# Performance work log

Measured on AMD Instinct MI355X. Metric: run time of the kernel, lower is better.

Reference implementation:

```python
import jax, jax.numpy as jnp
import numpy as np

N_NODES = 50000
N_EDGES = 1250000
D = 64
EPS = 1e-07


def setup_inputs() -> dict:
    key = jax.random.key(0)
    ks = jax.random.split(key, 10)
    return {
        "node_feats": jax.random.normal(ks[0], (N_NODES, D), jnp.float32),
        "emb0": jax.random.normal(ks[1], (8, D), jnp.float32),
        "emb1": jax.random.normal(ks[2], (4, D), jnp.float32),
        "W": jax.random.normal(ks[3], (D, D), jnp.float32) / np.sqrt(D),
        "b": jnp.zeros((D,), jnp.float32),
        "beta": jnp.ones((1,), jnp.float32),
        "scale": jnp.ones((1,), jnp.float32),
        "src": jax.random.randint(ks[4], (N_EDGES,), 0, N_NODES),
        "dst": jax.random.randint(ks[5], (N_EDGES,), 0, N_NODES),
        "edge_feat0": jax.random.randint(ks[6], (N_EDGES,), 0, 8),
        "edge_feat1": jax.random.randint(ks[7], (N_EDGES,), 0, 4),
    }


def reference(node_feats, emb0, emb1, W, b, beta, scale, src, dst, edge_feat0, edge_feat1):
    n = node_feats.shape[0]
    # edge embeddings summed over categorical feature types
    e = emb0[edge_feat0] + emb1[edge_feat1]              # [E, D]
    # u_add_e then relu + eps
    m = jnp.maximum(node_feats[src] + e, 0.0) + EPS      # [E, D]
    # edge softmax over edges sharing the same destination (per feature dim)
    logits = m * beta                                    # [E, D]
    mx = jax.ops.segment_max(logits, dst, num_segments=n)
    ex = jnp.exp(logits - mx[dst])
    denom = jax.ops.segment_sum(ex, dst, num_segments=n)
    a = ex / denom[dst]                                  # [E, D]
    # scatter-sum aggregation of m * a to destination nodes
    msg = jax.ops.segment_sum(m * a, dst, num_segments=n)  # [N, D]
    # MessageNorm: L2-normalize msg, rescale by ||node_feats|| * scale
    msg_unit = msg / jnp.maximum(
        jnp.linalg.norm(msg, axis=-1, keepdims=True), 1e-12)
    feats_norm = jnp.linalg.norm(node_feats, axis=-1, keepdims=True)
    msg = msg_unit * feats_norm * scale
    # residual + single-layer MLP
    feats = node_feats + msg
    return feats @ W + b
```

## Files before the change

### kernel.cpp

```cpp
#include <hip/hip_runtime.h>

#define NN 50000
#define NE 1250000
#define DD 64
#define KRF 1563
#define BSH 5
#define SCAPF 1024
#define SCSHF 10


__global__ __launch_bounds__(512) void k_part(
    const int4* __restrict__ src4, const int4* __restrict__ dst4,
    const int4* __restrict__ ef04, const int4* __restrict__ ef14,
    const float* __restrict__ W, float* __restrict__ Wt,
    int* __restrict__ rcur, unsigned* __restrict__ staging)
{
    __shared__ int hist[KRF], rbase[KRF], cur[KRF];
    const int t  = threadIdx.x;
    const int gb = blockIdx.x;

    for (int i = t; i < KRF; i += 512) { hist[i] = 0; cur[i] = 0; }
    if (gb == 0)
        for (int i = t; i < 4096; i += 512)
            Wt[(i & 63) * DD + (i >> 6)] = W[i];
    __syncthreads();

    unsigned pay[4];
    int rr[4];
#pragma unroll
    for (int u = 0; u < 4; ++u) rr[u] = -1;

    const int i4 = gb * 512 + t;
    if (i4 < NE / 4) {
        const int4 s  = src4[i4], d = dst4[i4];
        const int4 f0 = ef04[i4], f1 = ef14[i4];
        const int ds[4] = {d.x, d.y, d.z, d.w};
        const int ss[4] = {s.x, s.y, s.z, s.w};
        const int a0[4] = {f0.x, f0.y, f0.z, f0.w};
        const int a1[4] = {f1.x, f1.y, f1.z, f1.w};
#pragma unroll
        for (int u = 0; u < 4; ++u) {
            rr[u]  = ds[u] >> BSH;
            pay[u] = (unsigned)ss[u] | ((unsigned)(a1[u] * 8 + a0[u]) << 16)
                     | ((unsigned)(ds[u] & 31) << 21);
        }
    }
#pragma unroll
    for (int u = 0; u < 4; ++u)
        if (rr[u] >= 0) atomicAdd(&hist[rr[u]], 1);
    __syncthreads();

    for (int i = t; i < KRF; i += 512) {
        const int h = hist[i];
        if (h) rbase[i] = atomicAdd(&rcur[i], h);
    }
    __syncthreads();

#pragma unroll
    for (int u = 0; u < 4; ++u) {
        if (rr[u] >= 0) {
            const int r   = rr[u];
            const int pos = rbase[r] + atomicAdd(&cur[r], 1);
            if (pos < SCAPF) staging[(r << SCSHF) + pos] = pay[u];
        }
    }
}

__global__ __launch_bounds__(256, 4) void genconv_agg(
    const float* __restrict__ nf,
    const float* __restrict__ emb0, const float* __restrict__ emb1,
    const float* __restrict__ Wt,  const float* __restrict__ b,
    const float* __restrict__ beta_p, const float* __restrict__ scale_p,
    const unsigned* __restrict__ staging, const int* __restrict__ rcur,
    float* __restrict__ out)
{
    __shared__ float emb_s[32 * DD];
    __shared__ float feat_s[4][DD];
    __shared__ unsigned buck[32 * DD];
    __shared__ int ldeg[32];

    const int t    = threadIdx.x;
    const int w    = t >> 6;
    const int lane = t & 63;
    const int bin  = blockIdx.x;
    const int base_node = bin << BSH;

    if (t < 32) ldeg[t] = 0;
    for (int i = t; i < 32 * DD; i += 256) {
        const int rr = i >> 6, c = i & 63;
        emb_s[i] = emb0[(rr & 7) * DD + c] + emb1[(rr >> 3) * DD + c];
    }

    float4 wc[16];
#pragma unroll
    for (int k = 0; k < 16; ++k)
        wc[k] = *(const float4*)(Wt + lane * DD + 4 * k);

    const float bias  = b[lane];
    const float beta  = beta_p[0];
    const float scale = scale_p[0];
    __syncthreads();

    const int ne = min(rcur[bin], SCAPF);
    const unsigned* sg = staging + (bin << SCSHF);
    for (int i = t; i < ne; i += 256) {
        const unsigned p = sg[i];
        const int dl  = (p >> 21) & 31;
        const int pos = atomicAdd(&ldeg[dl], 1);
        if (pos < DD) buck[(dl << 6) + pos] = p & 0x1FFFFFu;
    }
    __syncthreads();

    const int nl0 = w << 3;
    unsigned pl = buck[(nl0 << 6) + lane];
    int cn = min(ldeg[nl0], DD);
    int node = base_node + nl0;
    float f = (node < NN) ? nf[(size_t)node * DD + lane] : 0.0f;

    for (int i = 0; i < 8; ++i) {
        const int nl = nl0 + i;
        node = base_node + nl;

        unsigned pl_n = 0u;
        int cn_n = 0;
        float f_n = 0.0f;
        if (i < 7) {
            pl_n = buck[((nl + 1) << 6) + lane];
            cn_n = ldeg[nl + 1];
            if (node + 1 < NN)
                f_n = nf[(size_t)(node + 1) * DD + lane];
        }

        float num = 0.0f, den = 0.0f;
        for (int j = 0; j < cn; j += 16) {
            float a[16];
            unsigned qv[16];
#pragma unroll
            for (int u = 0; u < 16; ++u) {
                const unsigned qq =
                    (unsigned)__builtin_amdgcn_readlane((int)pl, (j + u) & 63);
                qv[u] = qq;
                const int sidx = min((int)(qq & 0xFFFFu), NN - 1);
                a[u] = nf[(size_t)sidx * DD + lane];
            }
#pragma unroll
            for (int u = 0; u < 16; ++u) {
                const float eb = emb_s[(((qv[u] >> 16) & 31) << 6) + lane];
                const float m  = fmaxf(a[u] + eb, 0.0f) + 1e-7f;
                float x = __expf(beta * m);
                x = (j + u < cn) ? x : 0.0f;
                den += x;
                num = fmaf(m, x, num);
            }
        }

        const float msg = (den > 0.0f) ? num / den : 0.0f;

        float ss = msg * msg;
        float fs = f * f;
#pragma unroll
        for (int m = 32; m >= 1; m >>= 1) {
            ss += __shfl_xor(ss, m, 64);
            fs += __shfl_xor(fs, m, 64);
        }

        const float feat =
            f + msg * (1.0f / fmaxf(sqrtf(ss), 1e-12f)) * sqrtf(fs) * scale;

        feat_s[w][lane] = feat;

        float acc = bias;
#pragma unroll
        for (int k = 0; k < 16; ++k) {
            const float4 fv = *(const float4*)&feat_s[w][4 * k];
            acc = fmaf(fv.x, wc[k].x, acc);
            acc = fmaf(fv.y, wc[k].y, acc);
            acc = fmaf(fv.z, wc[k].z, acc);
            acc = fmaf(fv.w, wc[k].w, acc);
        }
        if (node < NN)
            out[(size_t)node * DD + lane] = acc;

        pl = pl_n;
        cn = min(cn_n, DD);
        f  = f_n;
    }
}

extern "C" void kernel_launch(void* const* d_in, const int* in_sizes, int n_in,
                              void* d_out, int out_size, void* d_ws, size_t ws_size,
                              hipStream_t stream)
{
    const float* nf    = (const float*)d_in[0];
    const float* emb0  = (const float*)d_in[1];
    const float* emb1  = (const float*)d_in[2];
    const float* W     = (const float*)d_in[3];
    const float* b     = (const float*)d_in[4];
    const float* beta  = (const float*)d_in[5];
    const float* scale = (const float*)d_in[6];
    const int* src = (const int*)d_in[7];
    const int* dst = (const int*)d_in[8];
    const int* ef0 = (const int*)d_in[9];
    const int* ef1 = (const int*)d_in[10];

    int*      rcur    = (int*)d_ws;
    float*    Wt      = (float*)(rcur + 2048);
    unsigned* staging = (unsigned*)(Wt + 4096);

    hipMemsetAsync(rcur, 0, 2048 * sizeof(int), stream);

    k_part<<<(NE / 4 + 511) / 512, 512, 0, stream>>>(
        (const int4*)src, (const int4*)dst, (const int4*)ef0, (const int4*)ef1,
        W, Wt, rcur, staging);

    genconv_agg<<<KRF, 256, 0, stream>>>(
        nf, emb0, emb1, Wt, b, beta, scale, staging, rcur, (float*)d_out);
}
```

Before: 201.1 us.

## Prefetch next node's first neighbor chunk and split masked/unmasked softmax paths

```diff
diff --git a/kernel.cpp b/kernel.cpp
--- a/kernel.cpp
+++ b/kernel.cpp
@@ -66,7 +66,7 @@
     }
 }
 
-__global__ __launch_bounds__(256, 4) void genconv_agg(
+__global__ __launch_bounds__(256, 2) void genconv_agg(
     const float* __restrict__ nf,
     const float* __restrict__ emb0, const float* __restrict__ emb1,
     const float* __restrict__ Wt,  const float* __restrict__ b,
@@ -114,25 +114,60 @@
     const int nl0 = w << 3;
     unsigned pl = buck[(nl0 << 6) + lane];
     int cn = min(ldeg[nl0], DD);
-    int node = base_node + nl0;
-    float f = (node < NN) ? nf[(size_t)node * DD + lane] : 0.0f;
+    float f;
+    {
+        const int node0 = base_node + nl0;
+        f = (node0 < NN) ? nf[(size_t)node0 * DD + lane] : 0.0f;
+    }
+
+    unsigned qp[16];
+    float ap[16];
+#pragma unroll
+    for (int u = 0; u < 16; ++u) {
+        const unsigned qq = (unsigned)__builtin_amdgcn_readlane((int)pl, u);
+        qp[u] = qq;
+        const int sidx = min((int)(qq & 0xFFFFu), NN - 1);
+        ap[u] = nf[(size_t)sidx * DD + lane];
+    }
 
     for (int i = 0; i < 8; ++i) {
         const int nl = nl0 + i;
-        node = base_node + nl;
+        const int node = base_node + nl;
 
         unsigned pl_n = 0u;
         int cn_n = 0;
         float f_n = 0.0f;
         if (i < 7) {
             pl_n = buck[((nl + 1) << 6) + lane];
-            cn_n = ldeg[nl + 1];
+            cn_n = min(ldeg[nl + 1], DD);
             if (node + 1 < NN)
                 f_n = nf[(size_t)(node + 1) * DD + lane];
         }
 
         float num = 0.0f, den = 0.0f;
-        for (int j = 0; j < cn; j += 16) {
+
+        if (cn >= 16) {
+#pragma unroll
+            for (int u = 0; u < 16; ++u) {
+                const float eb = emb_s[(((qp[u] >> 16) & 31) << 6) + lane];
+                const float m  = fmaxf(ap[u] + eb, 0.0f) + 1e-7f;
+                const float x  = __expf(beta * m);
+                den += x;
+                num = fmaf(m, x, num);
+            }
+        } else {
+#pragma unroll
+            for (int u = 0; u < 16; ++u) {
+                const float eb = emb_s[(((qp[u] >> 16) & 31) << 6) + lane];
+                const float m  = fmaxf(ap[u] + eb, 0.0f) + 1e-7f;
+                float x  = __expf(beta * m);
+                x = (u < cn) ? x : 0.0f;
+                den += x;
+                num = fmaf(m, x, num);
+            }
+        }
+
+        for (int j = 16; j < cn; j += 16) {
             float a[16];
             unsigned qv[16];
 #pragma unroll
@@ -143,14 +178,36 @@
                 const int sidx = min((int)(qq & 0xFFFFu), NN - 1);
                 a[u] = nf[(size_t)sidx * DD + lane];
             }
-#pragma unroll
-            for (int u = 0; u < 16; ++u) {
-                const float eb = emb_s[(((qv[u] >> 16) & 31) << 6) + lane];
-                const float m  = fmaxf(a[u] + eb, 0.0f) + 1e-7f;
-                float x = __expf(beta * m);
-                x = (j + u < cn) ? x : 0.0f;
-                den += x;
-                num = fmaf(m, x, num);
+            if (j + 16 <= cn) {
+#pragma unroll
+                for (int u = 0; u < 16; ++u) {
+                    const float eb = emb_s[(((qv[u] >> 16) & 31) << 6) + lane];
+                    const float m  = fmaxf(a[u] + eb, 0.0f) + 1e-7f;
+                    const float x  = __expf(beta * m);
+                    den += x;
+                    num = fmaf(m, x, num);
+                }
+            } else {
+#pragma unroll
+                for (int u = 0; u < 16; ++u) {
+                    const float eb = emb_s[(((qv[u] >> 16) & 31) << 6) + lane];
+                    const float m  = fmaxf(a[u] + eb, 0.0f) + 1e-7f;
+                    float x  = __expf(beta * m);
+                    x = (j + u < cn) ? x : 0.0f;
+                    den += x;
+                    num = fmaf(m, x, num);
+                }
+            }
+        }
+
+        if (i < 7) {
+#pragma unroll
+            for (int u = 0; u < 16; ++u) {
+                const unsigned qq =
+                    (unsigned)__builtin_amdgcn_readlane((int)pl_n, u);
+                qp[u] = qq;
+                const int sidx = min((int)(qq & 0xFFFFu), NN - 1);
+                ap[u] = nf[(size_t)sidx * DD + lane];
             }
         }
 
@@ -169,20 +226,31 @@
 
         feat_s[w][lane] = feat;
 
-        float acc = bias;
-#pragma unroll
-        for (int k = 0; k < 16; ++k) {
-            const float4 fv = *(const float4*)&feat_s[w][4 * k];
-            acc = fmaf(fv.x, wc[k].x, acc);
-            acc = fmaf(fv.y, wc[k].y, acc);
-            acc = fmaf(fv.z, wc[k].z, acc);
-            acc = fmaf(fv.w, wc[k].w, acc);
+        float ac0 = bias, ac1 = 0.0f, ac2 = 0.0f, ac3 = 0.0f;
+#pragma unroll
+        for (int k = 0; k < 4; ++k) {
+            const float4 fv0 = *(const float4*)&feat_s[w][16 * k];
+            const float4 fv1 = *(const float4*)&feat_s[w][16 * k + 4];
+            const float4 fv2 = *(const float4*)&feat_s[w][16 * k + 8];
+            const float4 fv3 = *(const float4*)&feat_s[w][16 * k + 12];
+            const float4 w0 = wc[4 * k];
+            const float4 w1 = wc[4 * k + 1];
+            const float4 w2 = wc[4 * k + 2];
+            const float4 w3 = wc[4 * k + 3];
+            ac0 = fmaf(fv0.x, w0.x, ac0); ac0 = fmaf(fv0.y, w0.y, ac0);
+            ac0 = fmaf(fv0.z, w0.z, ac0); ac0 = fmaf(fv0.w, w0.w, ac0);
+            ac1 = fmaf(fv1.x, w1.x, ac1); ac1 = fmaf(fv1.y, w1.y, ac1);
+            ac1 = fmaf(fv1.z, w1.z, ac1); ac1 = fmaf(fv1.w, w1.w, ac1);
+            ac2 = fmaf(fv2.x, w2.x, ac2); ac2 = fmaf(fv2.y, w2.y, ac2);
+            ac2 = fmaf(fv2.z, w2.z, ac2); ac2 = fmaf(fv2.w, w2.w, ac2);
+            ac3 = fmaf(fv3.x, w3.x, ac3); ac3 = fmaf(fv3.y, w3.y, ac3);
+            ac3 = fmaf(fv3.z, w3.z, ac3); ac3 = fmaf(fv3.w, w3.w, ac3);
         }
         if (node < NN)
-            out[(size_t)node * DD + lane] = acc;
+            out[(size_t)node * DD + lane] = (ac0 + ac1) + (ac2 + ac3);
 
         pl = pl_n;
-        cn = min(cn_n, DD);
+        cn = cn_n;
         f  = f_n;
     }
 }
```

Measured after the change: 214.7 us. 1.07x slower.

## Replace global-atomic bucket partition with count/scan/scatter passes

Applied to the files above, without the earlier changes.

```diff
diff --git a/kernel.cpp b/kernel.cpp
--- a/kernel.cpp
+++ b/kernel.cpp
@@ -7,28 +7,74 @@
 #define BSH 5
 #define SCAPF 1024
 #define SCSHF 10
-
-
-__global__ __launch_bounds__(512) void k_part(
-    const int4* __restrict__ src4, const int4* __restrict__ dst4,
-    const int4* __restrict__ ef04, const int4* __restrict__ ef14,
-    const float* __restrict__ W, float* __restrict__ Wt,
-    int* __restrict__ rcur, unsigned* __restrict__ staging)
-{
-    __shared__ int hist[KRF], rbase[KRF], cur[KRF];
+#define NBLK 611
+
+
+__global__ __launch_bounds__(512) void k_count(
+    const int4* __restrict__ dst4, unsigned short* __restrict__ hist,
+    const float* __restrict__ W, float* __restrict__ Wt)
+{
+    __shared__ int hs[KRF];
     const int t  = threadIdx.x;
     const int gb = blockIdx.x;
 
-    for (int i = t; i < KRF; i += 512) { hist[i] = 0; cur[i] = 0; }
+    for (int i = t; i < KRF; i += 512) hs[i] = 0;
     if (gb == 0)
         for (int i = t; i < 4096; i += 512)
             Wt[(i & 63) * DD + (i >> 6)] = W[i];
     __syncthreads();
 
-    unsigned pay[4];
-    int rr[4];
-#pragma unroll
-    for (int u = 0; u < 4; ++u) rr[u] = -1;
+    const int i4 = gb * 512 + t;
+    if (i4 < NE / 4) {
+        const int4 d = dst4[i4];
+        atomicAdd(&hs[d.x >> BSH], 1);
+        atomicAdd(&hs[d.y >> BSH], 1);
+        atomicAdd(&hs[d.z >> BSH], 1);
+        atomicAdd(&hs[d.w >> BSH], 1);
+    }
+    __syncthreads();
+
+    unsigned short* hrow = hist + (size_t)gb * KRF;
+    for (int i = t; i < KRF; i += 512)
+        hrow[i] = (unsigned short)hs[i];
+}
+
+__global__ __launch_bounds__(256) void k_scan(
+    unsigned short* __restrict__ hist, int* __restrict__ total)
+{
+    const int b = blockIdx.x * 256 + threadIdx.x;
+    if (b >= KRF) return;
+
+    int acc = 0;
+    for (int g0 = 0; g0 < NBLK; g0 += 16) {
+        const int n = min(16, NBLK - g0);
+        int hbuf[16];
+#pragma unroll
+        for (int k = 0; k < 16; ++k)
+            if (k < n) hbuf[k] = hist[(size_t)(g0 + k) * KRF + b];
+#pragma unroll
+        for (int k = 0; k < 16; ++k)
+            if (k < n) {
+                hist[(size_t)(g0 + k) * KRF + b] =
+                    (unsigned short)min(acc, 65535);
+                acc += hbuf[k];
+            }
+    }
+    total[b] = acc;
+}
+
+__global__ __launch_bounds__(512) void k_scatter(
+    const int4* __restrict__ src4, const int4* __restrict__ dst4,
+    const int4* __restrict__ ef04, const int4* __restrict__ ef14,
+    const unsigned short* __restrict__ hist, unsigned* __restrict__ staging)
+{
+    __shared__ int base_s[KRF], cur[KRF];
+    const int t  = threadIdx.x;
+    const int gb = blockIdx.x;
+
+    const unsigned short* hrow = hist + (size_t)gb * KRF;
+    for (int i = t; i < KRF; i += 512) { base_s[i] = hrow[i]; cur[i] = 0; }
+    __syncthreads();
 
     const int i4 = gb * 512 + t;
     if (i4 < NE / 4) {
@@ -40,28 +86,13 @@
         const int a1[4] = {f1.x, f1.y, f1.z, f1.w};
 #pragma unroll
         for (int u = 0; u < 4; ++u) {
-            rr[u]  = ds[u] >> BSH;
-            pay[u] = (unsigned)ss[u] | ((unsigned)(a1[u] * 8 + a0[u]) << 16)
-                     | ((unsigned)(ds[u] & 31) << 21);
-        }
-    }
-#pragma unroll
-    for (int u = 0; u < 4; ++u)
-        if (rr[u] >= 0) atomicAdd(&hist[rr[u]], 1);
-    __syncthreads();
-
-    for (int i = t; i < KRF; i += 512) {
-        const int h = hist[i];
-        if (h) rbase[i] = atomicAdd(&rcur[i], h);
-    }
-    __syncthreads();
-
-#pragma unroll
-    for (int u = 0; u < 4; ++u) {
-        if (rr[u] >= 0) {
-            const int r   = rr[u];
-            const int pos = rbase[r] + atomicAdd(&cur[r], 1);
-            if (pos < SCAPF) staging[(r << SCSHF) + pos] = pay[u];
+            const int bin = ds[u] >> BSH;
+            const unsigned pay = (unsigned)ss[u]
+                | ((unsigned)(a1[u] * 8 + a0[u]) << 16)
+                | ((unsigned)(ds[u] & 31) << 21);
+            const int rank = atomicAdd(&cur[bin], 1);
+            const int slot = base_s[bin] + rank;
+            if (slot < SCAPF) staging[(bin << SCSHF) + slot] = pay;
         }
     }
 }
@@ -71,7 +102,7 @@
     const float* __restrict__ emb0, const float* __restrict__ emb1,
     const float* __restrict__ Wt,  const float* __restrict__ b,
     const float* __restrict__ beta_p, const float* __restrict__ scale_p,
-    const unsigned* __restrict__ staging, const int* __restrict__ rcur,
+    const unsigned* __restrict__ staging, const int* __restrict__ total,
     float* __restrict__ out)
 {
     __shared__ float emb_s[32 * DD];
@@ -101,7 +132,7 @@
     const float scale = scale_p[0];
     __syncthreads();
 
-    const int ne = min(rcur[bin], SCAPF);
+    const int ne = min(total[bin], SCAPF);
     const unsigned* sg = staging + (bin << SCSHF);
     for (int i = t; i < ne; i += 256) {
         const unsigned p = sg[i];
@@ -203,16 +234,19 @@
     const int* ef0 = (const int*)d_in[9];
     const int* ef1 = (const int*)d_in[10];
 
-    int*      rcur    = (int*)d_ws;
-    float*    Wt      = (float*)(rcur + 2048);
-    unsigned* staging = (unsigned*)(Wt + 4096);
-
-    hipMemsetAsync(rcur, 0, 2048 * sizeof(int), stream);
-
-    k_part<<<(NE / 4 + 511) / 512, 512, 0, stream>>>(
+    int*            total   = (int*)d_ws;
+    float*          Wt      = (float*)(total + 2048);
+    unsigned*       staging = (unsigned*)(Wt + 4096);
+    unsigned short* hist    = (unsigned short*)(staging + (size_t)KRF * SCAPF);
+
+    k_count<<<NBLK, 512, 0, stream>>>((const int4*)dst, hist, W, Wt);
+
+    k_scan<<<(KRF + 255) / 256, 256, 0, stream>>>(hist, total);
+
+    k_scatter<<<NBLK, 512, 0, stream>>>(
         (const int4*)src, (const int4*)dst, (const int4*)ef0, (const int4*)ef1,
-        W, Wt, rcur, staging);
+        hist, staging);
 
     genconv_agg<<<KRF, 256, 0, stream>>>(
-        nf, emb0, emb1, Wt, b, beta, scale, staging, rcur, (float*)d_out);
-}
+        nf, emb0, emb1, Wt, b, beta, scale, staging, total, (float*)d_out);
+}
```

Result: slower. 231.4 us (+15.1%).
